# Performance work log

Hardware: AMD Instinct MI355X
Metric: run time of the kernel (lower is better)

Reference implementation:

```python
import jax, jax.numpy as jnp
import numpy as np

T, B, I, H = 512, 64, 1024, 1024
FORGET_BIAS = 1.0


def setup_inputs() -> dict:
    key = jax.random.key(0)
    ks = jax.random.split(key, 5)
    s = 0.02
    return {
        "x": jax.random.normal(ks[0], (T, B, I), dtype=jnp.float32),
        "Wx0": jax.random.normal(ks[1], (4 * H, I), dtype=jnp.float32) * s,
        "Wh0": jax.random.normal(ks[2], (4 * H, H), dtype=jnp.float32) * s,
        "Wx1": jax.random.normal(ks[3], (4 * H, H), dtype=jnp.float32) * s,
        "Wh1": jax.random.normal(ks[4], (4 * H, H), dtype=jnp.float32) * s,
    }


def _cell(x_t, h, c, Wx, Wh):
    # ifgo: [B, 4H]; gate chunk order in source is i, j, f, o
    ifgo = x_t @ Wx.T + h @ Wh.T
    i, j, f, o = jnp.split(ifgo, 4, axis=-1)
    c_next = c * jax.nn.sigmoid(f + FORGET_BIAS) + jax.nn.sigmoid(i) * jnp.tanh(j)
    h_next = jax.nn.sigmoid(o) * jnp.tanh(c_next)
    return h_next, c_next


def reference(x, Wx0, Wh0, Wx1, Wh1):
    b, hdim = x.shape[1], Wh0.shape[1]
    z = jnp.zeros((b, hdim), dtype=x.dtype)

    def step(carry, x_t):
        h0, c0, h1, c1 = carry
        h0, c0 = _cell(x_t, h0, c0, Wx0, Wh0)
        h1, c1 = _cell(h0, h1, c1, Wx1, Wh1)
        return (h0, c0, h1, c1), h1

    (h0, c0, h1, c1), out = jax.lax.scan(step, (z, z, z, z), x)
    h = jnp.stack([h0, h1])  # [n_layers, B, H]
    c = jnp.stack([c0, c1])
    return out, h, c
```

## Files before the change

### kernel.cpp

```cpp
#include <hip/hip_runtime.h>


#define T_STEPS 512
#define BATCH   64
#define HDIM    1024
#define KTOT    2048
#define BK      128
#define NITER   (KTOT / BK)
#define LDSTR   136
#define BH      (BATCH * HDIM)

typedef __bf16 bf16x8 __attribute__((ext_vector_type(8)));
typedef __bf16 bf16x4 __attribute__((ext_vector_type(4)));
typedef float  f32x4  __attribute__((ext_vector_type(4)));

__device__ __forceinline__ float sigm_(float x) { return 1.0f / (1.0f + __expf(-x)); }
__device__ __forceinline__ float tanh_(float x) {
    float e = __expf(-2.0f * fabsf(x));
    float t = (1.0f - e) / (1.0f + e);
    return copysignf(t, x);
}

__global__ __launch_bounds__(256) void lstm_step2(
    const __bf16* __restrict__ Ax0, const __bf16* __restrict__ Ah0,
    const __bf16* __restrict__ W0,  float* __restrict__ c0,
    __bf16* __restrict__ hb0, float* __restrict__ hf0, int en0,
    const __bf16* __restrict__ Ax1, const __bf16* __restrict__ Ah1,
    const __bf16* __restrict__ W1,  float* __restrict__ c1,
    __bf16* __restrict__ hb1, float* __restrict__ hf1, int en1)
{
    __shared__ __bf16 As[64 * LDSTR];
    __shared__ __bf16 Bs[64 * LDSTR];

    int bid = blockIdx.x;
    const __bf16 *Ax, *Ah, *W;
    float *c, *hf;
    __bf16 *hb;
    if (bid < 64) {
        if (!en0) return;
        Ax = Ax0; Ah = Ah0; W = W0; c = c0; hb = hb0; hf = hf0;
    } else {
        if (!en1) return;
        Ax = Ax1; Ah = Ah1; W = W1; c = c1; hb = hb1; hf = hf1; bid -= 64;
    }
    const int n0   = bid * 16;
    const int tid  = threadIdx.x;
    const int wave = tid >> 6;
    const int lane = tid & 63;
    const int sr   = tid >> 2;
    const int kc   = (tid & 3) * 32;
    const int wrow = (sr >> 4) * 1024 + n0 + (sr & 15);

    f32x4 acc[4] = {};

    bf16x8 pa[4], pb[4];
    {
        const __bf16* s = Ax + sr * 1024 + kc;
        #pragma unroll
        for (int u = 0; u < 4; ++u) pa[u] = *(const bf16x8*)(s + u * 8);
        const __bf16* w = W + wrow * 2048 + kc;
        #pragma unroll
        for (int u = 0; u < 4; ++u) pb[u] = *(const bf16x8*)(w + u * 8);
    }

    for (int it = 0; it < NITER; ++it) {
        #pragma unroll
        for (int u = 0; u < 4; ++u) *(bf16x8*)&As[sr * LDSTR + kc + u * 8] = pa[u];
        #pragma unroll
        for (int u = 0; u < 4; ++u) *(bf16x8*)&Bs[sr * LDSTR + kc + u * 8] = pb[u];
        __syncthreads();

        if (it + 1 < NITER) {
            int kb = (it + 1) * BK;
            const __bf16* s = (kb < 1024 ? Ax + sr * 1024 + kb
                                         : Ah + sr * 1024 + (kb - 1024)) + kc;
            #pragma unroll
            for (int u = 0; u < 4; ++u) pa[u] = *(const bf16x8*)(s + u * 8);
            const __bf16* w = W + wrow * 2048 + kb + kc;
            #pragma unroll
            for (int u = 0; u < 4; ++u) pb[u] = *(const bf16x8*)(w + u * 8);
        }

        const int lrow = lane & 15;
        const int lk   = (lane >> 4) * 8;
        #pragma unroll
        for (int s4 = 0; s4 < 4; ++s4) {
            bf16x8 af = *(bf16x8*)&As[(wave * 16 + lrow) * LDSTR + s4 * 32 + lk];
            #pragma unroll
            for (int g = 0; g < 4; ++g) {
                bf16x8 bf = *(bf16x8*)&Bs[(g * 16 + lrow) * LDSTR + s4 * 32 + lk];
                acc[g] = __builtin_amdgcn_mfma_f32_16x16x32_bf16(af, bf, acc[g], 0, 0, 0);
            }
        }
        __syncthreads();
    }

    const int n  = n0 + (lane & 15);
    const int mb = wave * 16 + (lane >> 4) * 4;
    #pragma unroll
    for (int r = 0; r < 4; ++r) {
        int m = mb + r;
        float gi = acc[0][r], gj = acc[1][r], gf = acc[2][r], go = acc[3][r];
        float cold = c[m * HDIM + n];
        float cn = cold * sigm_(gf + 1.0f) + sigm_(gi) * tanh_(gj);
        float hn = sigm_(go) * tanh_(cn);
        c[m * HDIM + n]  = cn;
        hb[m * HDIM + n] = (__bf16)hn;
        hf[m * HDIM + n] = hn;
    }
}

__global__ void convW(const float* __restrict__ Wx, const float* __restrict__ Wh,
                      __bf16* __restrict__ dst) {
    int i = blockIdx.x * 256 + threadIdx.x;
    int e = i * 4;
    int n = e >> 11;
    int k = e & 2047;
    const float* src = (k < 1024) ? (Wx + n * 1024 + k) : (Wh + n * 1024 + (k - 1024));
    float4 v = *(const float4*)src;
    bf16x4 o = { (__bf16)v.x, (__bf16)v.y, (__bf16)v.z, (__bf16)v.w };
    *(bf16x4*)(dst + e) = o;
}

__global__ void convX(const float* __restrict__ x, __bf16* __restrict__ dst) {
    int i = blockIdx.x * 256 + threadIdx.x;
    int e = i * 4;
    float4 v = *(const float4*)(x + e);
    bf16x4 o = { (__bf16)v.x, (__bf16)v.y, (__bf16)v.z, (__bf16)v.w };
    *(bf16x4*)(dst + e) = o;
}

__global__ void initz(__bf16* h0s, __bf16* h1s, float* c0, float* c1) {
    int i = blockIdx.x * 256 + threadIdx.x;
    h0s[i] = (__bf16)0.0f;
    h1s[i] = (__bf16)0.0f;
    c0[i] = 0.0f;
    c1[i] = 0.0f;
}

__global__ void epilogue_k(float* __restrict__ out, const float* __restrict__ h0f,
                           const float* __restrict__ c0, const float* __restrict__ c1) {
    int i = blockIdx.x * 256 + threadIdx.x;
    float* hout = out + (size_t)T_STEPS * BH;
    hout[i]      = h0f[i];
    hout[BH + i] = out[(size_t)(T_STEPS - 1) * BH + i];
    float* cout = hout + 2 * BH;
    cout[i]      = c0[i];
    cout[BH + i] = c1[i];
}

extern "C" void kernel_launch(void* const* d_in, const int* in_sizes, int n_in,
                              void* d_out, int out_size, void* d_ws, size_t ws_size,
                              hipStream_t stream) {
    const float* x   = (const float*)d_in[0];
    const float* Wx0 = (const float*)d_in[1];
    const float* Wh0 = (const float*)d_in[2];
    const float* Wx1 = (const float*)d_in[3];
    const float* Wh1 = (const float*)d_in[4];
    float* out = (float*)d_out;

    char* p = (char*)d_ws;
    __bf16* W0c = (__bf16*)p; p += (size_t)4096 * 2048 * 2;
    __bf16* W1c = (__bf16*)p; p += (size_t)4096 * 2048 * 2;
    __bf16* Xb  = (__bf16*)p; p += (size_t)T_STEPS * BH * 2;
    __bf16* h0s = (__bf16*)p; p += (size_t)2 * BH * 2;
    __bf16* h1s = (__bf16*)p; p += (size_t)2 * BH * 2;
    float*  c0v = (float*)p;  p += (size_t)BH * 4;
    float*  c1v = (float*)p;  p += (size_t)BH * 4;
    float*  h0f = (float*)p;  p += (size_t)BH * 4;

    convW<<<8192, 256, 0, stream>>>(Wx0, Wh0, W0c);
    convW<<<8192, 256, 0, stream>>>(Wx1, Wh1, W1c);
    convX<<<32768, 256, 0, stream>>>(x, Xb);
    initz<<<256, 256, 0, stream>>>(h0s, h1s, c0v, c1v);

    for (int s = 0; s <= T_STEPS; ++s) {
        int en0 = (s < T_STEPS);
        int en1 = (s >= 1);
        int t1  = en1 ? (s - 1) : 0;
        const __bf16* Ax0 = Xb + (size_t)(en0 ? s : 0) * BH;
        const __bf16* Ah0 = h0s + (size_t)(s & 1) * BH;
        __bf16*       hb0 = h0s + (size_t)((s & 1) ^ 1) * BH;
        const __bf16* Ax1 = h0s + (size_t)(s & 1) * BH;
        const __bf16* Ah1 = h1s + (size_t)(t1 & 1) * BH;
        __bf16*       hb1 = h1s + (size_t)((t1 & 1) ^ 1) * BH;
        float*        o1  = out + (size_t)t1 * BH;
        lstm_step2<<<128, 256, 0, stream>>>(Ax0, Ah0, W0c, c0v, hb0, h0f, en0,
                                            Ax1, Ah1, W1c, c1v, hb1, o1, en1);
    }

    epilogue_k<<<256, 256, 0, stream>>>(out, h0f, c0v, c1v);
}
```

Measured before the change: 10.50 ms.

## Replace per-step launches with persistent cooperative kernel holding weights in LDS

Replaces 513 per-timestep kernel launches with a single cooperative persistent kernel of 256 blocks that synchronise through a global atomic grid barrier. Each block loads its 16-row slice of both layers' bf16 weights into LDS once, about 132 KB, and reuses it for every step, so weights are no longer re-streamed from global memory each step. Cell state stays in registers, and the gate outputs are regrouped with wave shuffles. This removes launch overhead and weight traffic but adds barrier latency every step, depends on all blocks being co-resident, and needs a large shared-memory allocation per block.

New measurement: 33.64 ms. +220.5%, slower.

```diff
diff --git a/kernel.cpp b/kernel.cpp
--- a/kernel.cpp
+++ b/kernel.cpp
@@ -2,13 +2,12 @@
 
 
 #define T_STEPS 512
-#define BATCH   64
-#define HDIM    1024
-#define KTOT    2048
-#define BK      128
-#define NITER   (KTOT / BK)
-#define LDSTR   136
-#define BH      (BATCH * HDIM)
+#define BH      65536
+#define NBLK    256
+#define NTHR    512
+#define LDSTRW  2056
+#define WSLICE  (16 * LDSTRW)
+#define SMEM_BYTES (4 * WSLICE + 8192)
 
 typedef __bf16 bf16x8 __attribute__((ext_vector_type(8)));
 typedef __bf16 bf16x4 __attribute__((ext_vector_type(4)));
@@ -21,92 +20,163 @@
     return copysignf(t, x);
 }
 
-__global__ __launch_bounds__(256) void lstm_step2(
-    const __bf16* __restrict__ Ax0, const __bf16* __restrict__ Ah0,
-    const __bf16* __restrict__ W0,  float* __restrict__ c0,
-    __bf16* __restrict__ hb0, float* __restrict__ hf0, int en0,
-    const __bf16* __restrict__ Ax1, const __bf16* __restrict__ Ah1,
-    const __bf16* __restrict__ W1,  float* __restrict__ c1,
-    __bf16* __restrict__ hb1, float* __restrict__ hf1, int en1)
+__device__ __forceinline__ void gridbar(unsigned int* bar, unsigned int target) {
+    __threadfence();
+    __syncthreads();
+    if (threadIdx.x == 0) {
+        atomicAdd(bar, 1u);
+        while (__hip_atomic_load(bar, __ATOMIC_RELAXED, __HIP_MEMORY_SCOPE_AGENT) < target) {
+            __builtin_amdgcn_s_sleep(2);
+        }
+        __threadfence();
+    }
+    __syncthreads();
+}
+
+__global__ __launch_bounds__(NTHR, 2) void lstm_persist(
+    const __bf16* __restrict__ Xb,
+    const __bf16* __restrict__ W0,
+    const __bf16* __restrict__ W1,
+    float* __restrict__ out,
+    __bf16* __restrict__ h0b,
+    __bf16* __restrict__ h1b,
+    unsigned int* __restrict__ bar)
 {
-    __shared__ __bf16 As[64 * LDSTR];
-    __shared__ __bf16 Bs[64 * LDSTR];
-
-    int bid = blockIdx.x;
-    const __bf16 *Ax, *Ah, *W;
-    float *c, *hf;
-    __bf16 *hb;
-    if (bid < 64) {
-        if (!en0) return;
-        Ax = Ax0; Ah = Ah0; W = W0; c = c0; hb = hb0; hf = hf0;
-    } else {
-        if (!en1) return;
-        Ax = Ax1; Ah = Ah1; W = W1; c = c1; hb = hb1; hf = hf1; bid -= 64;
-    }
-    const int n0   = bid * 16;
-    const int tid  = threadIdx.x;
-    const int wave = tid >> 6;
-    const int lane = tid & 63;
-    const int sr   = tid >> 2;
-    const int kc   = (tid & 3) * 32;
-    const int wrow = (sr >> 4) * 1024 + n0 + (sr & 15);
-
-    f32x4 acc[4] = {};
-
-    bf16x8 pa[4], pb[4];
+    extern __shared__ char smem[];
+    __bf16* w0s = (__bf16*)smem;
+    __bf16* w1s = w0s + WSLICE;
+    float*  red = (float*)(smem + 4 * WSLICE);
+
+    const int tid = threadIdx.x;
+    const int bid = blockIdx.x;
+    const int w   = tid >> 6, l = tid & 63;
+    const int m   = w & 3;
+    const int kh  = w >> 2;
+    const int n0  = bid * 4;
+
+    for (int i = tid; i < 16 * 256; i += NTHR) {
+        int r  = i >> 8;
+        int ko = (i & 255) * 8;
+        size_t grow = (size_t)((r & 3) * 1024 + n0 + (r >> 2)) * 2048 + ko;
+        *(bf16x8*)&w0s[r * LDSTRW + ko] = *(const bf16x8*)&W0[grow];
+        *(bf16x8*)&w1s[r * LDSTRW + ko] = *(const bf16x8*)&W1[grow];
+    }
     {
-        const __bf16* s = Ax + sr * 1024 + kc;
-        #pragma unroll
-        for (int u = 0; u < 4; ++u) pa[u] = *(const bf16x8*)(s + u * 8);
-        const __bf16* w = W + wrow * 2048 + kc;
-        #pragma unroll
-        for (int u = 0; u < 4; ++u) pb[u] = *(const bf16x8*)(w + u * 8);
-    }
-
-    for (int it = 0; it < NITER; ++it) {
-        #pragma unroll
-        for (int u = 0; u < 4; ++u) *(bf16x8*)&As[sr * LDSTR + kc + u * 8] = pa[u];
-        #pragma unroll
-        for (int u = 0; u < 4; ++u) *(bf16x8*)&Bs[sr * LDSTR + kc + u * 8] = pb[u];
+        int idx = bid * NTHR + tid;
+        if (idx < 2 * BH / 8) {
+            bf16x8 z = {};
+            *(bf16x8*)&h0b[idx * 8] = z;
+            *(bf16x8*)&h1b[idx * 8] = z;
+        }
+    }
+    unsigned int epoch = 0;
+    gridbar(bar, ++epoch * NBLK);
+
+    float c0r = 0.f, c1r = 0.f, lh0 = 0.f, lh1 = 0.f;
+    const int arow = m * 16 + (l & 15);
+    const int lk8  = (l >> 4) * 8;
+    const int brow = (l & 15) * LDSTRW;
+
+    for (int s = 0; s <= T_STEPS; ++s) {
+        const bool en0 = (s < T_STEPS);
+        const bool en1 = (s >= 1);
+        const __bf16* h0p = h0b + ((s + 1) & 1) * BH;
+        const __bf16* h1p = h1b + (s & 1) * BH;
+        f32x4 a0 = {0.f, 0.f, 0.f, 0.f};
+        f32x4 a1 = {0.f, 0.f, 0.f, 0.f};
+        const int kb = kh * 512;
+
+        if (en0) {
+            const __bf16* xa = Xb + (size_t)s * BH + arow * 1024 + kb;
+            #pragma unroll
+            for (int kc = 0; kc < 16; ++kc) {
+                bf16x8 af = *(const bf16x8*)&xa[kc * 32 + lk8];
+                bf16x8 bf = *(const bf16x8*)&w0s[brow + kb + kc * 32 + lk8];
+                a0 = __builtin_amdgcn_mfma_f32_16x16x32_bf16(af, bf, a0, 0, 0, 0);
+            }
+        }
+        {
+            const __bf16* ha = h0p + arow * 1024 + kb;
+            const int o0 = brow + 1024 + kb;
+            const int o1 = brow + kb;
+            #pragma unroll
+            for (int kc = 0; kc < 16; ++kc) {
+                bf16x8 af = *(const bf16x8*)&ha[kc * 32 + lk8];
+                if (en0) {
+                    bf16x8 b0 = *(const bf16x8*)&w0s[o0 + kc * 32 + lk8];
+                    a0 = __builtin_amdgcn_mfma_f32_16x16x32_bf16(af, b0, a0, 0, 0, 0);
+                }
+                if (en1) {
+                    bf16x8 b1 = *(const bf16x8*)&w1s[o1 + kc * 32 + lk8];
+                    a1 = __builtin_amdgcn_mfma_f32_16x16x32_bf16(af, b1, a1, 0, 0, 0);
+                }
+            }
+        }
+        if (en1) {
+            const __bf16* ha = h1p + arow * 1024 + kb;
+            const int o1 = brow + 1024 + kb;
+            #pragma unroll
+            for (int kc = 0; kc < 16; ++kc) {
+                bf16x8 af = *(const bf16x8*)&ha[kc * 32 + lk8];
+                bf16x8 b1 = *(const bf16x8*)&w1s[o1 + kc * 32 + lk8];
+                a1 = __builtin_amdgcn_mfma_f32_16x16x32_bf16(af, b1, a1, 0, 0, 0);
+            }
+        }
+        if (kh == 1) {
+            *(f32x4*)&red[(m * 2 + 0) * 256 + l * 4] = a0;
+            *(f32x4*)&red[(m * 2 + 1) * 256 + l * 4] = a1;
+        }
         __syncthreads();
-
-        if (it + 1 < NITER) {
-            int kb = (it + 1) * BK;
-            const __bf16* s = (kb < 1024 ? Ax + sr * 1024 + kb
-                                         : Ah + sr * 1024 + (kb - 1024)) + kc;
-            #pragma unroll
-            for (int u = 0; u < 4; ++u) pa[u] = *(const bf16x8*)(s + u * 8);
-            const __bf16* w = W + wrow * 2048 + kb + kc;
-            #pragma unroll
-            for (int u = 0; u < 4; ++u) pb[u] = *(const bf16x8*)(w + u * 8);
-        }
-
-        const int lrow = lane & 15;
-        const int lk   = (lane >> 4) * 8;
-        #pragma unroll
-        for (int s4 = 0; s4 < 4; ++s4) {
-            bf16x8 af = *(bf16x8*)&As[(wave * 16 + lrow) * LDSTR + s4 * 32 + lk];
-            #pragma unroll
-            for (int g = 0; g < 4; ++g) {
-                bf16x8 bf = *(bf16x8*)&Bs[(g * 16 + lrow) * LDSTR + s4 * 32 + lk];
-                acc[g] = __builtin_amdgcn_mfma_f32_16x16x32_bf16(af, bf, acc[g], 0, 0, 0);
-            }
-        }
-        __syncthreads();
-    }
-
-    const int n  = n0 + (lane & 15);
-    const int mb = wave * 16 + (lane >> 4) * 4;
-    #pragma unroll
-    for (int r = 0; r < 4; ++r) {
-        int m = mb + r;
-        float gi = acc[0][r], gj = acc[1][r], gf = acc[2][r], go = acc[3][r];
-        float cold = c[m * HDIM + n];
-        float cn = cold * sigm_(gf + 1.0f) + sigm_(gi) * tanh_(gj);
-        float hn = sigm_(go) * tanh_(cn);
-        c[m * HDIM + n]  = cn;
-        hb[m * HDIM + n] = (__bf16)hn;
-        hf[m * HDIM + n] = hn;
+        if (kh == 0) {
+            a0 += *(const f32x4*)&red[(m * 2 + 0) * 256 + l * 4];
+            a1 += *(const f32x4*)&red[(m * 2 + 1) * 256 + l * 4];
+            const int q0  = (l & 48) | (l & 12);
+            const int col = n0 + ((l & 15) >> 2);
+            const int row = m * 16 + ((l >> 4) << 2) + (l & 3);
+            if (en0) {
+                #pragma unroll
+                for (int r = 0; r < 4; ++r) {
+                    float gi = __shfl(a0[r], q0);
+                    float gj = __shfl(a0[r], q0 | 1);
+                    float gf = __shfl(a0[r], q0 | 2);
+                    float go = __shfl(a0[r], q0 | 3);
+                    if ((l & 3) == r) {
+                        float cn = c0r * sigm_(gf + 1.0f) + sigm_(gi) * tanh_(gj);
+                        c0r = cn;
+                        float hn = sigm_(go) * tanh_(cn);
+                        lh0 = hn;
+                        h0b[(s & 1) * BH + row * 1024 + col] = (__bf16)hn;
+                    }
+                }
+            }
+            if (en1) {
+                #pragma unroll
+                for (int r = 0; r < 4; ++r) {
+                    float gi = __shfl(a1[r], q0);
+                    float gj = __shfl(a1[r], q0 | 1);
+                    float gf = __shfl(a1[r], q0 | 2);
+                    float go = __shfl(a1[r], q0 | 3);
+                    if ((l & 3) == r) {
+                        float cn = c1r * sigm_(gf + 1.0f) + sigm_(gi) * tanh_(gj);
+                        c1r = cn;
+                        float hn = sigm_(go) * tanh_(cn);
+                        lh1 = hn;
+                        h1b[((s + 1) & 1) * BH + row * 1024 + col] = (__bf16)hn;
+                        out[(size_t)(s - 1) * BH + row * 1024 + col] = hn;
+                    }
+                }
+            }
+        }
+        gridbar(bar, ++epoch * NBLK);
+    }
+    if (kh == 0) {
+        const int col = n0 + ((l & 15) >> 2);
+        const int row = m * 16 + ((l >> 4) << 2) + (l & 3);
+        float* hout = out + (size_t)T_STEPS * BH;
+        hout[row * 1024 + col]          = lh0;
+        hout[BH + row * 1024 + col]     = lh1;
+        hout[2 * BH + row * 1024 + col] = c0r;
+        hout[3 * BH + row * 1024 + col] = c1r;
     }
 }
 
@@ -130,25 +200,6 @@
     *(bf16x4*)(dst + e) = o;
 }
 
-__global__ void initz(__bf16* h0s, __bf16* h1s, float* c0, float* c1) {
-    int i = blockIdx.x * 256 + threadIdx.x;
-    h0s[i] = (__bf16)0.0f;
-    h1s[i] = (__bf16)0.0f;
-    c0[i] = 0.0f;
-    c1[i] = 0.0f;
-}
-
-__global__ void epilogue_k(float* __restrict__ out, const float* __restrict__ h0f,
-                           const float* __restrict__ c0, const float* __restrict__ c1) {
-    int i = blockIdx.x * 256 + threadIdx.x;
-    float* hout = out + (size_t)T_STEPS * BH;
-    hout[i]      = h0f[i];
-    hout[BH + i] = out[(size_t)(T_STEPS - 1) * BH + i];
-    float* cout = hout + 2 * BH;
-    cout[i]      = c0[i];
-    cout[BH + i] = c1[i];
-}
-
 extern "C" void kernel_launch(void* const* d_in, const int* in_sizes, int n_in,
                               void* d_out, int out_size, void* d_ws, size_t ws_size,
                               hipStream_t stream) {
@@ -163,31 +214,20 @@
     __bf16* W0c = (__bf16*)p; p += (size_t)4096 * 2048 * 2;
     __bf16* W1c = (__bf16*)p; p += (size_t)4096 * 2048 * 2;
     __bf16* Xb  = (__bf16*)p; p += (size_t)T_STEPS * BH * 2;
-    __bf16* h0s = (__bf16*)p; p += (size_t)2 * BH * 2;
-    __bf16* h1s = (__bf16*)p; p += (size_t)2 * BH * 2;
-    float*  c0v = (float*)p;  p += (size_t)BH * 4;
-    float*  c1v = (float*)p;  p += (size_t)BH * 4;
-    float*  h0f = (float*)p;  p += (size_t)BH * 4;
+    __bf16* h0b = (__bf16*)p; p += (size_t)2 * BH * 2;
+    __bf16* h1b = (__bf16*)p; p += (size_t)2 * BH * 2;
+    unsigned int* bar = (unsigned int*)p; p += 128;
 
     convW<<<8192, 256, 0, stream>>>(Wx0, Wh0, W0c);
     convW<<<8192, 256, 0, stream>>>(Wx1, Wh1, W1c);
     convX<<<32768, 256, 0, stream>>>(x, Xb);
-    initz<<<256, 256, 0, stream>>>(h0s, h1s, c0v, c1v);
-
-    for (int s = 0; s <= T_STEPS; ++s) {
-        int en0 = (s < T_STEPS);
-        int en1 = (s >= 1);
-        int t1  = en1 ? (s - 1) : 0;
-        const __bf16* Ax0 = Xb + (size_t)(en0 ? s : 0) * BH;
-        const __bf16* Ah0 = h0s + (size_t)(s & 1) * BH;
-        __bf16*       hb0 = h0s + (size_t)((s & 1) ^ 1) * BH;
-        const __bf16* Ax1 = h0s + (size_t)(s & 1) * BH;
-        const __bf16* Ah1 = h1s + (size_t)(t1 & 1) * BH;
-        __bf16*       hb1 = h1s + (size_t)((t1 & 1) ^ 1) * BH;
-        float*        o1  = out + (size_t)t1 * BH;
-        lstm_step2<<<128, 256, 0, stream>>>(Ax0, Ah0, W0c, c0v, hb0, h0f, en0,
-                                            Ax1, Ah1, W1c, c1v, hb1, o1, en1);
-    }
-
-    epilogue_k<<<256, 256, 0, stream>>>(out, h0f, c0v, c1v);
-}
+    hipMemsetAsync(bar, 0, 128, stream);
+
+    hipFuncSetAttribute((const void*)lstm_persist,
+                        hipFuncAttributeMaxDynamicSharedMemorySize, SMEM_BYTES);
+
+    void* args[] = { (void*)&Xb, (void*)&W0c, (void*)&W1c, (void*)&out,
+                     (void*)&h0b, (void*)&h1b, (void*)&bar };
+    hipLaunchCooperativeKernel((void*)lstm_persist, dim3(NBLK), dim3(NTHR),
+                               args, SMEM_BYTES, stream);
+}
```
